# Optimization experiments

Hardware: AMD Instinct MI355X
Metric: run time of the kernel (lower is better)

The kernel has to match this reference:

```python
import jax, jax.numpy as jnp
import numpy as np

B, T, D = 2, 512, 512
UNITS, H = 512, 8
DEPTH = UNITS // H  # 64


def setup_inputs() -> dict:
    key = jax.random.key(0)
    ks = jax.random.split(key, 16)
    s = 0.05  # keras 'random_normal' initializer stddev
    inp = {
        "query": jax.random.normal(ks[0], (B, T, D), jnp.float32),
        "key": jax.random.normal(ks[1], (B, T, D), jnp.float32),
        "value": jax.random.normal(ks[2], (B, T, D), jnp.float32),
        # input projections (Dense(units) with bias)
        "Wq": jax.random.normal(ks[3], (D, UNITS), jnp.float32) * s,
        "bq": jnp.zeros((UNITS,), jnp.float32),
        "Wk": jax.random.normal(ks[4], (D, UNITS), jnp.float32) * s,
        "bk": jnp.zeros((UNITS,), jnp.float32),
        "Wv": jax.random.normal(ks[5], (D, UNITS), jnp.float32) * s,
        "bv": jnp.zeros((UNITS,), jnp.float32),
        # per-head additive-attention params, stacked over heads
        "Wq_h": jax.random.normal(ks[6], (H, DEPTH, DEPTH), jnp.float32) * s,
        "Wk_h": jax.random.normal(ks[7], (H, DEPTH, DEPTH), jnp.float32) * s,
        "va_h": jax.random.normal(ks[8], (H, DEPTH), jnp.float32) * s,
        "b_h": jnp.zeros((H, DEPTH), jnp.float32),
        # output projection
        "Wo": jax.random.normal(ks[9], (UNITS, UNITS), jnp.float32) * s,
        "bo": jnp.zeros((UNITS,), jnp.float32),
    }
    return inp


def _split_heads(x):
    b = x.shape[0]
    return x.reshape(b, -1, H, DEPTH).transpose(0, 2, 1, 3)  # [B,H,T,depth]


def reference(query, key, value, Wq, bq, Wk, bk, Wv, bv,
              Wq_h, Wk_h, va_h, b_h, Wo, bo):
    Q = _split_heads(query @ Wq + bq)  # [B,H,T,d]
    K = _split_heads(key @ Wk + bk)    # [B,H,S,d]
    V = _split_heads(value @ Wv + bv)  # computed but unused, as in original

    # per-head linear maps for additive scores
    q = jnp.einsum("bhtd,hde->bhte", Q, Wq_h)
    k = jnp.einsum("bhsd,hde->bhse", K, Wk_h)
    # Bahdanau additive score: tanh(q_t + k_s + b) . v_a, summed over depth
    feat = jnp.tanh(q[:, :, :, None, :] + k[:, :, None, :, :]
                    + b_h[None, :, None, None, :])  # [B,H,T,S,d]
    score = jnp.einsum("bhtse,he->bhts", feat, va_h)  # [B,H,T,S]
    attn = jax.nn.softmax(score, axis=-1)
    # original multiplies by KEY (not value)
    heads = jnp.einsum("bhts,bhsd->bhtd", attn, K)  # [B,H,T,d]
    merged = heads.transpose(0, 2, 1, 3).reshape(query.shape[0], -1, UNITS)
    return merged @ Wo + bo
```

## Files before the change

kernel.cpp:

```cpp
#include <hip/hip_runtime.h>
#include <hip/hip_bf16.h>

#define T_SEQ 512
#define NH 8
#define DEPTH 64
#define UNITS_ 512
#define SCALE2 2.8853900817779268f
#define LOG2E 1.4426950408889634f

typedef __attribute__((ext_vector_type(8))) short short8;
typedef __attribute__((ext_vector_type(4))) float floatx4;

__global__ __launch_bounds__(256) void gemm64(
    const float* __restrict__ A0, const float* __restrict__ W0,
    const float* __restrict__ bias0, float* __restrict__ C0,
    const float* __restrict__ A1, const float* __restrict__ W1,
    const float* __restrict__ bias1, float* __restrict__ C1)
{
    const float* A = blockIdx.z ? A1 : A0;
    const float* W = blockIdx.z ? W1 : W0;
    const float* bias = blockIdx.z ? bias1 : bias0;
    float* C = blockIdx.z ? C1 : C0;

    __shared__ float As[32][68];
    __shared__ float Bs[32][68];

    const int tid = threadIdx.x;
    const int m0 = blockIdx.y * 64;
    const int n0 = blockIdx.x * 64;

    const int arow = tid >> 2;
    const int acol = (tid & 3) * 8;
    const int bk = tid >> 3;
    const int bn = (tid & 7) * 8;

    const int ti = tid >> 4;
    const int tj = tid & 15;

    float4 acc[4];
    acc[0] = acc[1] = acc[2] = acc[3] = make_float4(0.f, 0.f, 0.f, 0.f);

    for (int k0 = 0; k0 < 512; k0 += 32) {
        float4 av0 = *(const float4*)&A[(m0 + arow) * 512 + k0 + acol];
        float4 av1 = *(const float4*)&A[(m0 + arow) * 512 + k0 + acol + 4];
        float4 bv0 = *(const float4*)&W[(k0 + bk) * 512 + n0 + bn];
        float4 bv1 = *(const float4*)&W[(k0 + bk) * 512 + n0 + bn + 4];
        __syncthreads();
        As[acol + 0][arow] = av0.x;
        As[acol + 1][arow] = av0.y;
        As[acol + 2][arow] = av0.z;
        As[acol + 3][arow] = av0.w;
        As[acol + 4][arow] = av1.x;
        As[acol + 5][arow] = av1.y;
        As[acol + 6][arow] = av1.z;
        As[acol + 7][arow] = av1.w;
        *(float4*)&Bs[bk][bn] = bv0;
        *(float4*)&Bs[bk][bn + 4] = bv1;
        __syncthreads();
        #pragma unroll
        for (int kk = 0; kk < 32; ++kk) {
            float4 a4 = *(const float4*)&As[kk][4 * ti];
            float4 b4 = *(const float4*)&Bs[kk][4 * tj];
            acc[0].x = fmaf(a4.x, b4.x, acc[0].x);
            acc[0].y = fmaf(a4.x, b4.y, acc[0].y);
            acc[0].z = fmaf(a4.x, b4.z, acc[0].z);
            acc[0].w = fmaf(a4.x, b4.w, acc[0].w);
            acc[1].x = fmaf(a4.y, b4.x, acc[1].x);
            acc[1].y = fmaf(a4.y, b4.y, acc[1].y);
            acc[1].z = fmaf(a4.y, b4.z, acc[1].z);
            acc[1].w = fmaf(a4.y, b4.w, acc[1].w);
            acc[2].x = fmaf(a4.z, b4.x, acc[2].x);
            acc[2].y = fmaf(a4.z, b4.y, acc[2].y);
            acc[2].z = fmaf(a4.z, b4.z, acc[2].z);
            acc[2].w = fmaf(a4.z, b4.w, acc[2].w);
            acc[3].x = fmaf(a4.w, b4.x, acc[3].x);
            acc[3].y = fmaf(a4.w, b4.y, acc[3].y);
            acc[3].z = fmaf(a4.w, b4.z, acc[3].z);
            acc[3].w = fmaf(a4.w, b4.w, acc[3].w);
        }
    }
    float4 bb = *(const float4*)&bias[n0 + 4 * tj];
    #pragma unroll
    for (int r = 0; r < 4; ++r) {
        float4 o;
        float4 a = acc[r];
        o.x = a.x + bb.x; o.y = a.y + bb.y; o.z = a.z + bb.z; o.w = a.w + bb.w;
        *(float4*)&C[(m0 + 4 * ti + r) * 512 + n0 + 4 * tj] = o;
    }
}

__global__ __launch_bounds__(256) void head_xform(
    const float* __restrict__ Qb, const float* __restrict__ Kb,
    const float* __restrict__ Wq_h, const float* __restrict__ Wk_h,
    const float* __restrict__ bh,
    float* __restrict__ eq, float* __restrict__ ekT,
    __hip_bfloat16* __restrict__ KhT)
{
    __shared__ float As[64][68];
    __shared__ float Ws[64][68];

    const int tid = threadIdx.x;
    const int t0 = blockIdx.x * 64;
    const int h = blockIdx.y;
    const int which = blockIdx.z & 1;
    const int b = blockIdx.z >> 1;
    const int bh_i = b * NH + h;

    const float* In = which ? Kb : Qb;
    const float* Wp = (which ? Wk_h : Wq_h) + h * 64 * 64;

    const int e4 = (tid & 15) * 4;
    const int tr = tid >> 4;

    #pragma unroll
    for (int r = 0; r < 4; ++r) {
        const int t = tr + 16 * r;
        float4 v = *(const float4*)&In[(b * 512 + t0 + t) * 512 + h * 64 + e4];
        As[e4 + 0][t] = v.x;
        As[e4 + 1][t] = v.y;
        As[e4 + 2][t] = v.z;
        As[e4 + 3][t] = v.w;
        *(float4*)&Ws[t][e4] = *(const float4*)&Wp[t * 64 + e4];
    }
    __syncthreads();

    const int ti = tid >> 4;
    const int tj = tid & 15;
    float4 acc[4];
    acc[0] = acc[1] = acc[2] = acc[3] = make_float4(0.f, 0.f, 0.f, 0.f);
    #pragma unroll 8
    for (int d = 0; d < 64; ++d) {
        float4 a4 = *(const float4*)&As[d][4 * ti];
        float4 b4 = *(const float4*)&Ws[d][4 * tj];
        acc[0].x = fmaf(a4.x, b4.x, acc[0].x);
        acc[0].y = fmaf(a4.x, b4.y, acc[0].y);
        acc[0].z = fmaf(a4.x, b4.z, acc[0].z);
        acc[0].w = fmaf(a4.x, b4.w, acc[0].w);
        acc[1].x = fmaf(a4.y, b4.x, acc[1].x);
        acc[1].y = fmaf(a4.y, b4.y, acc[1].y);
        acc[1].z = fmaf(a4.y, b4.z, acc[1].z);
        acc[1].w = fmaf(a4.y, b4.w, acc[1].w);
        acc[2].x = fmaf(a4.z, b4.x, acc[2].x);
        acc[2].y = fmaf(a4.z, b4.y, acc[2].y);
        acc[2].z = fmaf(a4.z, b4.z, acc[2].z);
        acc[2].w = fmaf(a4.z, b4.w, acc[2].w);
        acc[3].x = fmaf(a4.w, b4.x, acc[3].x);
        acc[3].y = fmaf(a4.w, b4.y, acc[3].y);
        acc[3].z = fmaf(a4.w, b4.z, acc[3].z);
        acc[3].w = fmaf(a4.w, b4.w, acc[3].w);
    }

    if (which == 0) {
        float* outp = eq + (bh_i * 512 + t0) * 64;
        #pragma unroll
        for (int r = 0; r < 4; ++r) {
            float4 o;
            o.x = __builtin_amdgcn_exp2f(SCALE2 * acc[r].x);
            o.y = __builtin_amdgcn_exp2f(SCALE2 * acc[r].y);
            o.z = __builtin_amdgcn_exp2f(SCALE2 * acc[r].z);
            o.w = __builtin_amdgcn_exp2f(SCALE2 * acc[r].w);
            *(float4*)&outp[(4 * ti + r) * 64 + 4 * tj] = o;
        }
        return;
    }

    float4 bhv = *(const float4*)&bh[h * 64 + 4 * tj];
    __syncthreads();
    #pragma unroll
    for (int r = 0; r < 4; ++r) {
        Ws[4 * tj + 0][4 * ti + r] = __builtin_amdgcn_exp2f(SCALE2 * (acc[r].x + bhv.x));
        Ws[4 * tj + 1][4 * ti + r] = __builtin_amdgcn_exp2f(SCALE2 * (acc[r].y + bhv.y));
        Ws[4 * tj + 2][4 * ti + r] = __builtin_amdgcn_exp2f(SCALE2 * (acc[r].z + bhv.z));
        Ws[4 * tj + 3][4 * ti + r] = __builtin_amdgcn_exp2f(SCALE2 * (acc[r].w + bhv.w));
    }
    __syncthreads();

    const int dd = tid >> 2;
    const int sc = (tid & 3) * 16;
    float* ekp = ekT + ((size_t)bh_i * 64 + dd) * 512 + t0 + sc;
    #pragma unroll
    for (int c = 0; c < 4; ++c)
        *(float4*)&ekp[4 * c] = *(float4*)&Ws[dd][sc + 4 * c];

    __hip_bfloat16* kp = KhT + ((size_t)bh_i * 64 + dd) * 512 + t0 + sc;
    union { short8 v; short s[8]; } pk0, pk1;
    #pragma unroll
    for (int i = 0; i < 8; ++i) {
        __hip_bfloat16 b0 = __hip_bfloat16(As[dd][sc + i]);
        __hip_bfloat16 b1 = __hip_bfloat16(As[dd][sc + 8 + i]);
        pk0.s[i] = *(short*)&b0;
        pk1.s[i] = *(short*)&b1;
    }
    *(short8*)kp = pk0.v;
    *(short8*)(kp + 8) = pk1.v;
}

__global__ __launch_bounds__(512, 4) void attn_v2(
    const float* __restrict__ eq, const float* __restrict__ ekT,
    const __hip_bfloat16* __restrict__ KhT, const float* __restrict__ va_h,
    float* __restrict__ merged)
{
    __shared__ __hip_bfloat16 pA[16][520];
    __shared__ float wsum[16][8];

    const int tid = threadIdx.x;
    const int w = tid >> 6;
    const int l = tid & 63;
    const int t0 = blockIdx.x * 16;
    const int h = blockIdx.y;
    const int b = blockIdx.z;
    const int bh_i = b * NH + h;

    const float* eq_p = eq + ((size_t)bh_i * 512 + t0) * 64;
    const float* ekT_p = ekT + (size_t)bh_i * 64 * 512 + tid;
    const float* va_p = va_h + h * 64;

    float acc[16];
    #pragma unroll
    for (int t = 0; t < 16; ++t) acc[t] = 0.f;

    #pragma unroll
    for (int e0 = 0; e0 < 64; e0 += 16) {
        float ekv[16];
        #pragma unroll
        for (int j = 0; j < 16; ++j) ekv[j] = ekT_p[(e0 + j) * 512];
        float nv[16];
        #pragma unroll
        for (int j = 0; j < 16; ++j) nv[j] = -2.0f * va_p[e0 + j];
        #pragma unroll
        for (int t = 0; t < 16; ++t) {
            float a = acc[t];
            #pragma unroll
            for (int q = 0; q < 4; ++q) {
                float4 e4 = *(const float4*)&eq_p[t * 64 + e0 + q * 4];
                a = fmaf(nv[q * 4 + 0], __builtin_amdgcn_rcpf(fmaf(e4.x, ekv[q * 4 + 0], 1.0f)), a);
                a = fmaf(nv[q * 4 + 1], __builtin_amdgcn_rcpf(fmaf(e4.y, ekv[q * 4 + 1], 1.0f)), a);
                a = fmaf(nv[q * 4 + 2], __builtin_amdgcn_rcpf(fmaf(e4.z, ekv[q * 4 + 2], 1.0f)), a);
                a = fmaf(nv[q * 4 + 3], __builtin_amdgcn_rcpf(fmaf(e4.w, ekv[q * 4 + 3], 1.0f)), a);
            }
            acc[t] = a;
        }
    }

    float ev[16];
    #pragma unroll
    for (int t = 0; t < 16; ++t) {
        float s = __builtin_amdgcn_exp2f(acc[t] * LOG2E);
        ev[t] = s;
        #pragma unroll
        for (int off = 32; off > 0; off >>= 1) s += __shfl_xor(s, off, 64);
        if (l == 0) wsum[t][w] = s;
    }
    __syncthreads();
    #pragma unroll
    for (int t = 0; t < 16; ++t) {
        float4 s0 = *(float4*)&wsum[t][0];
        float4 s1 = *(float4*)&wsum[t][4];
        float inv = 1.0f / (((s0.x + s0.y) + (s0.z + s0.w)) + ((s1.x + s1.y) + (s1.z + s1.w)));
        pA[t][tid] = __hip_bfloat16(ev[t] * inv);
    }
    __syncthreads();

    if (w < 4) {
        const __hip_bfloat16* kp = KhT + (size_t)bh_i * 64 * 512
                                   + ((size_t)(w * 16 + (l & 15))) * 512 + (l >> 4) * 8;
        const __hip_bfloat16* ap = &pA[l & 15][(l >> 4) * 8];
        floatx4 oacc = {0.f, 0.f, 0.f, 0.f};
        #pragma unroll
        for (int kt = 0; kt < 16; ++kt) {
            short8 af = *(const short8*)(ap + kt * 32);
            short8 bf = *(const short8*)(kp + kt * 32);
            oacc = __builtin_amdgcn_mfma_f32_16x16x32_bf16(af, bf, oacc, 0, 0, 0);
        }
        const int row = (l >> 4) * 4;
        const int col = w * 16 + (l & 15);
        float* mp = merged + ((size_t)(b * 512 + t0 + row)) * 512 + h * 64 + col;
        #pragma unroll
        for (int r = 0; r < 4; ++r) mp[r * 512] = oacc[r];
    }
}

extern "C" void kernel_launch(void* const* d_in, const int* in_sizes, int n_in,
                              void* d_out, int out_size, void* d_ws, size_t ws_size,
                              hipStream_t stream) {
    (void)in_sizes; (void)n_in; (void)out_size; (void)ws_size;
    const float* query = (const float*)d_in[0];
    const float* key   = (const float*)d_in[1];
    const float* Wq   = (const float*)d_in[3];
    const float* bq   = (const float*)d_in[4];
    const float* Wk   = (const float*)d_in[5];
    const float* bk   = (const float*)d_in[6];
    const float* Wq_h = (const float*)d_in[9];
    const float* Wk_h = (const float*)d_in[10];
    const float* va_h = (const float*)d_in[11];
    const float* b_h  = (const float*)d_in[12];
    const float* Wo   = (const float*)d_in[13];
    const float* bo   = (const float*)d_in[14];

    float* out = (float*)d_out;
    float* ws = (float*)d_ws;
    const int SZ = 1024 * 512;
    float* Qb      = ws;
    float* Kb      = Qb + SZ;
    float* eqb     = Kb + SZ;
    float* ekTb    = eqb + SZ;
    float* mergedb = ekTb + SZ;
    __hip_bfloat16* KhTb = (__hip_bfloat16*)(mergedb + SZ);

    gemm64<<<dim3(8, 16, 2), 256, 0, stream>>>(query, Wq, bq, Qb,
                                               key, Wk, bk, Kb);
    head_xform<<<dim3(8, 8, 4), 256, 0, stream>>>(Qb, Kb, Wq_h, Wk_h, b_h,
                                                  eqb, ekTb, KhTb);
    attn_v2<<<dim3(32, 8, 2), 512, 0, stream>>>(eqb, ekTb, KhTb, va_h, mergedb);
    gemm64<<<dim3(8, 16, 1), 256, 0, stream>>>(mergedb, Wo, bo, out,
                                               mergedb, Wo, bo, out);
}
```

Before: 192.1 us.

## Fold per-head weights into projections and use split-bf16 MFMA GEMMs

Precomputes the effective weights Wq·Wq_h and Wk·Wk_h, plus the matching biases, so the head transform no longer needs its own pass and the Q/K projections write eq, ekT and KhT directly from the GEMM epilogue. It replaces the fp32 FMA GEMMs with MFMA bf16 GEMMs that use a hi/lo split (three products) to keep close to fp32 accuracy, with the weights pre-transposed and pre-split in prep kernels. The attention kernel now loads all ek values up front and broadcasts eq and va across lanes with readlane instead of reloading them. This adds weight-preparation kernels on every call and needs more registers in attention.

New measurement: 285.4 us. +48.5%, slower.

```diff
diff --git a/kernel.cpp b/kernel.cpp
--- a/kernel.cpp
+++ b/kernel.cpp
@@ -1,137 +1,104 @@
 #include <hip/hip_runtime.h>
 #include <hip/hip_bf16.h>
 
-#define T_SEQ 512
 #define NH 8
-#define DEPTH 64
-#define UNITS_ 512
 #define SCALE2 2.8853900817779268f
 #define LOG2E 1.4426950408889634f
 
 typedef __attribute__((ext_vector_type(8))) short short8;
 typedef __attribute__((ext_vector_type(4))) float floatx4;
 
-__global__ __launch_bounds__(256) void gemm64(
-    const float* __restrict__ A0, const float* __restrict__ W0,
-    const float* __restrict__ bias0, float* __restrict__ C0,
-    const float* __restrict__ A1, const float* __restrict__ W1,
-    const float* __restrict__ bias1, float* __restrict__ C1)
-{
-    const float* A = blockIdx.z ? A1 : A0;
-    const float* W = blockIdx.z ? W1 : W0;
-    const float* bias = blockIdx.z ? bias1 : bias0;
-    float* C = blockIdx.z ? C1 : C0;
-
-    __shared__ float As[32][68];
-    __shared__ float Bs[32][68];
-
-    const int tid = threadIdx.x;
-    const int m0 = blockIdx.y * 64;
-    const int n0 = blockIdx.x * 64;
-
-    const int arow = tid >> 2;
-    const int acol = (tid & 3) * 8;
-    const int bk = tid >> 3;
-    const int bn = (tid & 7) * 8;
-
-    const int ti = tid >> 4;
-    const int tj = tid & 15;
-
-    float4 acc[4];
-    acc[0] = acc[1] = acc[2] = acc[3] = make_float4(0.f, 0.f, 0.f, 0.f);
-
-    for (int k0 = 0; k0 < 512; k0 += 32) {
-        float4 av0 = *(const float4*)&A[(m0 + arow) * 512 + k0 + acol];
-        float4 av1 = *(const float4*)&A[(m0 + arow) * 512 + k0 + acol + 4];
-        float4 bv0 = *(const float4*)&W[(k0 + bk) * 512 + n0 + bn];
-        float4 bv1 = *(const float4*)&W[(k0 + bk) * 512 + n0 + bn + 4];
-        __syncthreads();
-        As[acol + 0][arow] = av0.x;
-        As[acol + 1][arow] = av0.y;
-        As[acol + 2][arow] = av0.z;
-        As[acol + 3][arow] = av0.w;
-        As[acol + 4][arow] = av1.x;
-        As[acol + 5][arow] = av1.y;
-        As[acol + 6][arow] = av1.z;
-        As[acol + 7][arow] = av1.w;
-        *(float4*)&Bs[bk][bn] = bv0;
-        *(float4*)&Bs[bk][bn + 4] = bv1;
-        __syncthreads();
-        #pragma unroll
-        for (int kk = 0; kk < 32; ++kk) {
-            float4 a4 = *(const float4*)&As[kk][4 * ti];
-            float4 b4 = *(const float4*)&Bs[kk][4 * tj];
-            acc[0].x = fmaf(a4.x, b4.x, acc[0].x);
-            acc[0].y = fmaf(a4.x, b4.y, acc[0].y);
-            acc[0].z = fmaf(a4.x, b4.z, acc[0].z);
-            acc[0].w = fmaf(a4.x, b4.w, acc[0].w);
-            acc[1].x = fmaf(a4.y, b4.x, acc[1].x);
-            acc[1].y = fmaf(a4.y, b4.y, acc[1].y);
-            acc[1].z = fmaf(a4.y, b4.z, acc[1].z);
-            acc[1].w = fmaf(a4.y, b4.w, acc[1].w);
-            acc[2].x = fmaf(a4.z, b4.x, acc[2].x);
-            acc[2].y = fmaf(a4.z, b4.y, acc[2].y);
-            acc[2].z = fmaf(a4.z, b4.z, acc[2].z);
-            acc[2].w = fmaf(a4.z, b4.w, acc[2].w);
-            acc[3].x = fmaf(a4.w, b4.x, acc[3].x);
-            acc[3].y = fmaf(a4.w, b4.y, acc[3].y);
-            acc[3].z = fmaf(a4.w, b4.z, acc[3].z);
-            acc[3].w = fmaf(a4.w, b4.w, acc[3].w);
-        }
-    }
-    float4 bb = *(const float4*)&bias[n0 + 4 * tj];
-    #pragma unroll
-    for (int r = 0; r < 4; ++r) {
-        float4 o;
-        float4 a = acc[r];
-        o.x = a.x + bb.x; o.y = a.y + bb.y; o.z = a.z + bb.z; o.w = a.w + bb.w;
-        *(float4*)&C[(m0 + 4 * ti + r) * 512 + n0 + 4 * tj] = o;
-    }
-}
-
-__global__ __launch_bounds__(256) void head_xform(
-    const float* __restrict__ Qb, const float* __restrict__ Kb,
+__device__ __forceinline__ void split2(float v, unsigned short& hi, unsigned short& lo) {
+    __hip_bfloat16 h = __hip_bfloat16(v);
+    float hf = (float)h;
+    __hip_bfloat16 l = __hip_bfloat16(v - hf);
+    hi = *(unsigned short*)&h;
+    lo = *(unsigned short*)&l;
+}
+
+__device__ __forceinline__ float rdlane(float v, int lane) {
+    return __int_as_float(__builtin_amdgcn_readlane(__float_as_int(v), lane));
+}
+
+__device__ __forceinline__ void cvt8(float4 a, float4 b, short8& hi8, short8& lo8) {
+    union { short8 v; unsigned short u[8]; } H, L;
+    split2(a.x, H.u[0], L.u[0]);
+    split2(a.y, H.u[1], L.u[1]);
+    split2(a.z, H.u[2], L.u[2]);
+    split2(a.w, H.u[3], L.u[3]);
+    split2(b.x, H.u[4], L.u[4]);
+    split2(b.y, H.u[5], L.u[5]);
+    split2(b.z, H.u[6], L.u[6]);
+    split2(b.w, H.u[7], L.u[7]);
+    hi8 = H.v; lo8 = L.v;
+}
+
+__global__ __launch_bounds__(256) void prep_transpose(
+    const float* __restrict__ Wk, const float* __restrict__ Wo,
+    unsigned short* __restrict__ WkTh, unsigned short* __restrict__ WkTl,
+    unsigned short* __restrict__ WoTh, unsigned short* __restrict__ WoTl)
+{
+    __shared__ unsigned short Th[64][72];
+    __shared__ unsigned short Tl[64][72];
+    const int z = blockIdx.z;
+    const float* W = z ? Wo : Wk;
+    unsigned short* Oh = z ? WoTh : WkTh;
+    unsigned short* Ol = z ? WoTl : WkTl;
+    const int k0 = blockIdx.x * 64, n0 = blockIdx.y * 64;
+    const int tid = threadIdx.x;
+    const int rr = tid >> 4, c4 = (tid & 15) * 4;
+    #pragma unroll
+    for (int j = 0; j < 4; ++j) {
+        const int r = rr + 16 * j;
+        float4 v = *(const float4*)&W[(size_t)(k0 + r) * 512 + n0 + c4];
+        split2(v.x, Th[c4 + 0][r], Tl[c4 + 0][r]);
+        split2(v.y, Th[c4 + 1][r], Tl[c4 + 1][r]);
+        split2(v.z, Th[c4 + 2][r], Tl[c4 + 2][r]);
+        split2(v.w, Th[c4 + 3][r], Tl[c4 + 3][r]);
+    }
+    __syncthreads();
+    const int nl = tid >> 2, kc = (tid & 3) * 16;
+    const size_t ob = (size_t)(n0 + nl) * 512 + k0 + kc;
+    *(short8*)&Oh[ob] = *(short8*)&Th[nl][kc];
+    *(short8*)&Oh[ob + 8] = *(short8*)&Th[nl][kc + 8];
+    *(short8*)&Ol[ob] = *(short8*)&Tl[nl][kc];
+    *(short8*)&Ol[ob + 8] = *(short8*)&Tl[nl][kc + 8];
+}
+
+__global__ __launch_bounds__(256) void prep_weff(
+    const float* __restrict__ Wq, const float* __restrict__ Wk,
     const float* __restrict__ Wq_h, const float* __restrict__ Wk_h,
-    const float* __restrict__ bh,
-    float* __restrict__ eq, float* __restrict__ ekT,
-    __hip_bfloat16* __restrict__ KhT)
+    unsigned short* __restrict__ WqeTh, unsigned short* __restrict__ WqeTl,
+    unsigned short* __restrict__ WkeTh, unsigned short* __restrict__ WkeTl)
 {
     __shared__ float As[64][68];
-    __shared__ float Ws[64][68];
-
-    const int tid = threadIdx.x;
-    const int t0 = blockIdx.x * 64;
-    const int h = blockIdx.y;
-    const int which = blockIdx.z & 1;
-    const int b = blockIdx.z >> 1;
-    const int bh_i = b * NH + h;
-
-    const float* In = which ? Kb : Qb;
-    const float* Wp = (which ? Wk_h : Wq_h) + h * 64 * 64;
-
-    const int e4 = (tid & 15) * 4;
-    const int tr = tid >> 4;
-
-    #pragma unroll
-    for (int r = 0; r < 4; ++r) {
-        const int t = tr + 16 * r;
-        float4 v = *(const float4*)&In[(b * 512 + t0 + t) * 512 + h * 64 + e4];
-        As[e4 + 0][t] = v.x;
-        As[e4 + 1][t] = v.y;
-        As[e4 + 2][t] = v.z;
-        As[e4 + 3][t] = v.w;
-        *(float4*)&Ws[t][e4] = *(const float4*)&Wp[t * 64 + e4];
+    __shared__ float Bs[64][68];
+    const int tid = threadIdx.x;
+    const int k0 = blockIdx.x * 64, h = blockIdx.y, qk = blockIdx.z;
+    const float* W = qk ? Wk : Wq;
+    const float* Wh = (qk ? Wk_h : Wq_h) + h * 4096;
+    unsigned short* Th = qk ? WkeTh : WqeTh;
+    unsigned short* Tl = qk ? WkeTl : WqeTl;
+
+    const int rr = tid >> 4, d4 = (tid & 15) * 4;
+    #pragma unroll
+    for (int j = 0; j < 4; ++j) {
+        const int r = rr + 16 * j;
+        float4 v = *(const float4*)&W[(size_t)(k0 + r) * 512 + h * 64 + d4];
+        As[d4 + 0][r] = v.x;
+        As[d4 + 1][r] = v.y;
+        As[d4 + 2][r] = v.z;
+        As[d4 + 3][r] = v.w;
+        *(float4*)&Bs[r][d4] = *(const float4*)&Wh[r * 64 + d4];
     }
     __syncthreads();
-
-    const int ti = tid >> 4;
-    const int tj = tid & 15;
+    const int ti = tid >> 4, tj = tid & 15;
     float4 acc[4];
     acc[0] = acc[1] = acc[2] = acc[3] = make_float4(0.f, 0.f, 0.f, 0.f);
     #pragma unroll 8
     for (int d = 0; d < 64; ++d) {
         float4 a4 = *(const float4*)&As[d][4 * ti];
-        float4 b4 = *(const float4*)&Ws[d][4 * tj];
+        float4 b4 = *(const float4*)&Bs[d][4 * tj];
         acc[0].x = fmaf(a4.x, b4.x, acc[0].x);
         acc[0].y = fmaf(a4.x, b4.y, acc[0].y);
         acc[0].z = fmaf(a4.x, b4.z, acc[0].z);
@@ -149,94 +116,175 @@
         acc[3].z = fmaf(a4.w, b4.z, acc[3].z);
         acc[3].w = fmaf(a4.w, b4.w, acc[3].w);
     }
-
-    if (which == 0) {
-        float* outp = eq + (bh_i * 512 + t0) * 64;
+    #pragma unroll
+    for (int c = 0; c < 4; ++c) {
+        union { ushort4 v; unsigned short u[4]; } H, L;
         #pragma unroll
         for (int r = 0; r < 4; ++r) {
-            float4 o;
-            o.x = __builtin_amdgcn_exp2f(SCALE2 * acc[r].x);
-            o.y = __builtin_amdgcn_exp2f(SCALE2 * acc[r].y);
-            o.z = __builtin_amdgcn_exp2f(SCALE2 * acc[r].z);
-            o.w = __builtin_amdgcn_exp2f(SCALE2 * acc[r].w);
-            *(float4*)&outp[(4 * ti + r) * 64 + 4 * tj] = o;
-        }
-        return;
-    }
-
-    float4 bhv = *(const float4*)&bh[h * 64 + 4 * tj];
-    __syncthreads();
-    #pragma unroll
-    for (int r = 0; r < 4; ++r) {
-        Ws[4 * tj + 0][4 * ti + r] = __builtin_amdgcn_exp2f(SCALE2 * (acc[r].x + bhv.x));
-        Ws[4 * tj + 1][4 * ti + r] = __builtin_amdgcn_exp2f(SCALE2 * (acc[r].y + bhv.y));
-        Ws[4 * tj + 2][4 * ti + r] = __builtin_amdgcn_exp2f(SCALE2 * (acc[r].z + bhv.z));
-        Ws[4 * tj + 3][4 * ti + r] = __builtin_amdgcn_exp2f(SCALE2 * (acc[r].w + bhv.w));
-    }
-    __syncthreads();
-
-    const int dd = tid >> 2;
-    const int sc = (tid & 3) * 16;
-    float* ekp = ekT + ((size_t)bh_i * 64 + dd) * 512 + t0 + sc;
-    #pragma unroll
-    for (int c = 0; c < 4; ++c)
-        *(float4*)&ekp[4 * c] = *(float4*)&Ws[dd][sc + 4 * c];
-
-    __hip_bfloat16* kp = KhT + ((size_t)bh_i * 64 + dd) * 512 + t0 + sc;
-    union { short8 v; short s[8]; } pk0, pk1;
-    #pragma unroll
-    for (int i = 0; i < 8; ++i) {
-        __hip_bfloat16 b0 = __hip_bfloat16(As[dd][sc + i]);
-        __hip_bfloat16 b1 = __hip_bfloat16(As[dd][sc + 8 + i]);
-        pk0.s[i] = *(short*)&b0;
-        pk1.s[i] = *(short*)&b1;
-    }
-    *(short8*)kp = pk0.v;
-    *(short8*)(kp + 8) = pk1.v;
-}
-
-__global__ __launch_bounds__(512, 4) void attn_v2(
+            float val = c == 0 ? acc[r].x : c == 1 ? acc[r].y : c == 2 ? acc[r].z : acc[r].w;
+            split2(val, H.u[r], L.u[r]);
+        }
+        const size_t ob = (size_t)(h * 64 + 4 * tj + c) * 512 + k0 + 4 * ti;
+        *(ushort4*)&Th[ob] = H.v;
+        *(ushort4*)&Tl[ob] = L.v;
+    }
+}
+
+__global__ __launch_bounds__(512) void prep_bias(
+    const float* __restrict__ bq, const float* __restrict__ bk,
+    const float* __restrict__ Wq_h, const float* __restrict__ Wk_h,
+    const float* __restrict__ b_h,
+    float* __restrict__ bqe, float* __restrict__ bke)
+{
+    const int tid = threadIdx.x;
+    const int h = tid >> 6, e = tid & 63;
+    float aq = 0.f, ak = 0.f;
+    for (int d = 0; d < 64; ++d) {
+        aq = fmaf(bq[h * 64 + d], Wq_h[(h * 64 + d) * 64 + e], aq);
+        ak = fmaf(bk[h * 64 + d], Wk_h[(h * 64 + d) * 64 + e], ak);
+    }
+    bqe[tid] = aq;
+    bke[tid] = ak + b_h[tid];
+}
+
+__global__ __launch_bounds__(256, 2) void gemm_split(
+    const float* __restrict__ Aq, const float* __restrict__ Akey,
+    const unsigned short* __restrict__ W0h, const unsigned short* __restrict__ W0l,
+    const unsigned short* __restrict__ W1h, const unsigned short* __restrict__ W1l,
+    const unsigned short* __restrict__ W2h, const unsigned short* __restrict__ W2l,
+    const float* __restrict__ bias0, const float* __restrict__ bias1,
+    const float* __restrict__ bias2,
+    float* __restrict__ out0, float* __restrict__ ekT,
+    unsigned short* __restrict__ KhT, int mode_ofs)
+{
+    const int mode = blockIdx.z + mode_ofs;
+    const float* A = (mode == 1 || mode == 2) ? Akey : Aq;
+    const unsigned short* Wh = (mode == 1) ? W1h : (mode == 2) ? W2h : W0h;
+    const unsigned short* Wl = (mode == 1) ? W1l : (mode == 2) ? W2l : W0l;
+    const float* bias = (mode == 1) ? bias1 : (mode == 2) ? bias2 : bias0;
+
+    const int tid = threadIdx.x;
+    const int wv = tid >> 6, l = tid & 63;
+    const int lr = l & 15, lq = l >> 4;
+    const int m0 = blockIdx.y * 64 + (wv & 1) * 32;
+    const int n0 = blockIdx.x * 64 + (wv >> 1) * 32;
+
+    const size_t aoff0 = (size_t)(m0 + lr) * 512 + lq * 8;
+    const size_t aoff1 = aoff0 + (size_t)16 * 512;
+    const size_t boff0 = (size_t)(n0 + lr) * 512 + lq * 8;
+    const size_t boff1 = boff0 + (size_t)16 * 512;
+
+    floatx4 acc[2][2];
+    #pragma unroll
+    for (int i = 0; i < 2; ++i)
+        #pragma unroll
+        for (int j = 0; j < 2; ++j)
+            acc[i][j] = (floatx4){0.f, 0.f, 0.f, 0.f};
+
+    #pragma unroll
+    for (int k0 = 0; k0 < 512; k0 += 64) {
+        short8 ah[2][2], al[2][2], bh8[2][2], bl8[2][2];
+        #pragma unroll
+        for (int i = 0; i < 2; ++i) {
+            #pragma unroll
+            for (int c = 0; c < 2; ++c) {
+                const float* ap = A + (i ? aoff1 : aoff0) + k0 + c * 32;
+                float4 a0 = *(const float4*)ap;
+                float4 a1 = *(const float4*)(ap + 4);
+                cvt8(a0, a1, ah[i][c], al[i][c]);
+                const size_t bo = (i ? boff1 : boff0) + k0 + c * 32;
+                bh8[i][c] = *(const short8*)&Wh[bo];
+                bl8[i][c] = *(const short8*)&Wl[bo];
+            }
+        }
+        #pragma unroll
+        for (int i = 0; i < 2; ++i)
+            #pragma unroll
+            for (int j = 0; j < 2; ++j)
+                #pragma unroll
+                for (int c = 0; c < 2; ++c) {
+                    acc[i][j] = __builtin_amdgcn_mfma_f32_16x16x32_bf16(ah[i][c], bh8[j][c], acc[i][j], 0, 0, 0);
+                    acc[i][j] = __builtin_amdgcn_mfma_f32_16x16x32_bf16(ah[i][c], bl8[j][c], acc[i][j], 0, 0, 0);
+                    acc[i][j] = __builtin_amdgcn_mfma_f32_16x16x32_bf16(al[i][c], bh8[j][c], acc[i][j], 0, 0, 0);
+                }
+    }
+
+    #pragma unroll
+    for (int i = 0; i < 2; ++i) {
+        #pragma unroll
+        for (int j = 0; j < 2; ++j) {
+            const int n = n0 + j * 16 + lr;
+            const float bv = bias[n];
+            #pragma unroll
+            for (int r = 0; r < 4; ++r) {
+                const int m = m0 + i * 16 + lq * 4 + r;
+                float v = acc[i][j][r] + bv;
+                if (mode == 0) {
+                    v = __builtin_amdgcn_exp2f(SCALE2 * v);
+                    out0[(size_t)((m >> 9) * 8 + (n >> 6)) * 32768 + (size_t)(m & 511) * 64 + (n & 63)] = v;
+                } else if (mode == 1) {
+                    v = __builtin_amdgcn_exp2f(SCALE2 * v);
+                    ekT[((size_t)((m >> 9) * 8 + (n >> 6)) * 64 + (n & 63)) * 512 + (m & 511)] = v;
+                } else if (mode == 2) {
+                    __hip_bfloat16 hb(v);
+                    KhT[((size_t)((m >> 9) * 8 + (n >> 6)) * 64 + (n & 63)) * 512 + (m & 511)] = *(unsigned short*)&hb;
+                } else {
+                    out0[(size_t)m * 512 + n] = v;
+                }
+            }
+        }
+    }
+}
+
+__global__ __launch_bounds__(512, 4) void attn_v3(
     const float* __restrict__ eq, const float* __restrict__ ekT,
-    const __hip_bfloat16* __restrict__ KhT, const float* __restrict__ va_h,
+    const unsigned short* __restrict__ KhT, const float* __restrict__ va_h,
     float* __restrict__ merged)
 {
     __shared__ __hip_bfloat16 pA[16][520];
     __shared__ float wsum[16][8];
 
     const int tid = threadIdx.x;
-    const int w = tid >> 6;
-    const int l = tid & 63;
-    const int t0 = blockIdx.x * 16;
-    const int h = blockIdx.y;
-    const int b = blockIdx.z;
+    const int w = tid >> 6, l = tid & 63;
+    const int t0 = blockIdx.x * 16, h = blockIdx.y, b = blockIdx.z;
     const int bh_i = b * NH + h;
 
-    const float* eq_p = eq + ((size_t)bh_i * 512 + t0) * 64;
-    const float* ekT_p = ekT + (size_t)bh_i * 64 * 512 + tid;
+    const float* eq_p = eq + (size_t)bh_i * 32768 + (size_t)t0 * 64;
+    const float* ekT_p = ekT + (size_t)bh_i * 32768 + tid;
     const float* va_p = va_h + h * 64;
 
+    float4 eqv[4];
+    #pragma unroll
+    for (int j = 0; j < 4; ++j) eqv[j] = *(const float4*)&eq_p[l * 16 + 4 * j];
+    float4 va4 = *(const float4*)&va_p[(l & 15) * 4];
+    va4.x *= -2.0f; va4.y *= -2.0f; va4.z *= -2.0f; va4.w *= -2.0f;
+    float ekv[64];
+    #pragma unroll
+    for (int j = 0; j < 64; ++j) ekv[j] = ekT_p[(size_t)j * 512];
+
     float acc[16];
     #pragma unroll
     for (int t = 0; t < 16; ++t) acc[t] = 0.f;
 
     #pragma unroll
     for (int e0 = 0; e0 < 64; e0 += 16) {
-        float ekv[16];
-        #pragma unroll
-        for (int j = 0; j < 16; ++j) ekv[j] = ekT_p[(e0 + j) * 512];
-        float nv[16];
-        #pragma unroll
-        for (int j = 0; j < 16; ++j) nv[j] = -2.0f * va_p[e0 + j];
+        float nva[16];
+        #pragma unroll
+        for (int j = 0; j < 16; ++j) {
+            const int e = e0 + j;
+            float c = (j & 3) == 0 ? va4.x : (j & 3) == 1 ? va4.y : (j & 3) == 2 ? va4.z : va4.w;
+            nva[j] = rdlane(c, e >> 2);
+        }
         #pragma unroll
         for (int t = 0; t < 16; ++t) {
+            const int lt = 4 * t + (e0 >> 4);
             float a = acc[t];
             #pragma unroll
-            for (int q = 0; q < 4; ++q) {
-                float4 e4 = *(const float4*)&eq_p[t * 64 + e0 + q * 4];
-                a = fmaf(nv[q * 4 + 0], __builtin_amdgcn_rcpf(fmaf(e4.x, ekv[q * 4 + 0], 1.0f)), a);
-                a = fmaf(nv[q * 4 + 1], __builtin_amdgcn_rcpf(fmaf(e4.y, ekv[q * 4 + 1], 1.0f)), a);
-                a = fmaf(nv[q * 4 + 2], __builtin_amdgcn_rcpf(fmaf(e4.z, ekv[q * 4 + 2], 1.0f)), a);
-                a = fmaf(nv[q * 4 + 3], __builtin_amdgcn_rcpf(fmaf(e4.w, ekv[q * 4 + 3], 1.0f)), a);
+            for (int j = 0; j < 16; ++j) {
+                const int q = j >> 2, s3 = j & 3;
+                float comp = s3 == 0 ? eqv[q].x : s3 == 1 ? eqv[q].y : s3 == 2 ? eqv[q].z : eqv[q].w;
+                float eqs = rdlane(comp, lt);
+                a = fmaf(nva[j], __builtin_amdgcn_rcpf(fmaf(eqs, ekv[e0 + j], 1.0f)), a);
             }
             acc[t] = a;
         }
@@ -262,7 +310,7 @@
     __syncthreads();
 
     if (w < 4) {
-        const __hip_bfloat16* kp = KhT + (size_t)bh_i * 64 * 512
+        const unsigned short* kp = KhT + (size_t)bh_i * 32768
                                    + ((size_t)(w * 16 + (l & 15))) * 512 + (l >> 4) * 8;
         const __hip_bfloat16* ap = &pA[l & 15][(l >> 4) * 8];
         floatx4 oacc = {0.f, 0.f, 0.f, 0.f};
@@ -296,22 +344,34 @@
     const float* b_h  = (const float*)d_in[12];
     const float* Wo   = (const float*)d_in[13];
     const float* bo   = (const float*)d_in[14];
-
     float* out = (float*)d_out;
+
     float* ws = (float*)d_ws;
-    const int SZ = 1024 * 512;
-    float* Qb      = ws;
-    float* Kb      = Qb + SZ;
-    float* eqb     = Kb + SZ;
-    float* ekTb    = eqb + SZ;
-    float* mergedb = ekTb + SZ;
-    __hip_bfloat16* KhTb = (__hip_bfloat16*)(mergedb + SZ);
-
-    gemm64<<<dim3(8, 16, 2), 256, 0, stream>>>(query, Wq, bq, Qb,
-                                               key, Wk, bk, Kb);
-    head_xform<<<dim3(8, 8, 4), 256, 0, stream>>>(Qb, Kb, Wq_h, Wk_h, b_h,
-                                                  eqb, ekTb, KhTb);
-    attn_v2<<<dim3(32, 8, 2), 512, 0, stream>>>(eqb, ekTb, KhTb, va_h, mergedb);
-    gemm64<<<dim3(8, 16, 1), 256, 0, stream>>>(mergedb, Wo, bo, out,
-                                               mergedb, Wo, bo, out);
-}
+    float* eqb     = ws;
+    float* ekTb    = eqb + 524288;
+    float* mergedb = ekTb + 524288;
+    float* bqe     = mergedb + 524288;
+    float* bke     = bqe + 512;
+    unsigned short* u = (unsigned short*)(bke + 512);
+    unsigned short* WqeTh = u;             u += 262144;
+    unsigned short* WqeTl = u;             u += 262144;
+    unsigned short* WkeTh = u;             u += 262144;
+    unsigned short* WkeTl = u;             u += 262144;
+    unsigned short* WkTh  = u;             u += 262144;
+    unsigned short* WkTl  = u;             u += 262144;
+    unsigned short* WoTh  = u;             u += 262144;
+    unsigned short* WoTl  = u;             u += 262144;
+    unsigned short* KhTb  = u;             u += 524288;
+
+    prep_transpose<<<dim3(8, 8, 2), 256, 0, stream>>>(Wk, Wo, WkTh, WkTl, WoTh, WoTl);
+    prep_weff<<<dim3(8, 8, 2), 256, 0, stream>>>(Wq, Wk, Wq_h, Wk_h,
+                                                 WqeTh, WqeTl, WkeTh, WkeTl);
+    prep_bias<<<1, 512, 0, stream>>>(bq, bk, Wq_h, Wk_h, b_h, bqe, bke);
+    gemm_split<<<dim3(8, 16, 3), 256, 0, stream>>>(
+        query, key, WqeTh, WqeTl, WkeTh, WkeTl, WkTh, WkTl,
+        bqe, bke, bk, eqb, ekTb, KhTb, 0);
+    attn_v3<<<dim3(32, 8, 2), 512, 0, stream>>>(eqb, ekTb, KhTb, va_h, mergedb);
+    gemm_split<<<dim3(8, 16, 1), 256, 0, stream>>>(
+        mergedb, mergedb, WoTh, WoTl, WoTh, WoTl, WoTh, WoTl,
+        bo, bo, bo, out, ekTb, KhTb, 3);
+}
```
